# Optimization experiments

Hardware: AMD Instinct MI355X
Metric: run time of the kernel (lower is better)

## Reference

```python
import jax, jax.numpy as jnp
import numpy as np

HIDDEN = 768
HEADS = 12
HEAD_DIM = HIDDEN // HEADS  # 64


def setup_inputs() -> dict:
    key = jax.random.key(0)
    k1, k2, k3 = jax.random.split(key, 3)
    B, N, C = 64, 197, HIDDEN
    hidden_states = jax.random.normal(k1, (B, N, C), dtype=jnp.float32)
    # qkv Linear: weight [C, 3C] (stored transposed for x @ W), bias [3C]
    w_qkv = jax.random.normal(k2, (C, 3 * C), dtype=jnp.float32) * (1.0 / np.sqrt(C))
    b_qkv = jax.random.normal(k3, (3 * C,), dtype=jnp.float32) * 0.02
    return {"hidden_states": hidden_states, "w_qkv": w_qkv, "b_qkv": b_qkv}


def reference(hidden_states, w_qkv, b_qkv):
    B, N, C = hidden_states.shape
    scale = HEAD_DIM ** -0.5
    qkv = hidden_states @ w_qkv + b_qkv                      # [B, N, 3C]
    qkv = qkv.reshape(B, N, 3, HEADS, HEAD_DIM)
    qkv = jnp.transpose(qkv, (2, 0, 3, 1, 4))                # [3, B, H, N, d]
    q, k, v = qkv[0], qkv[1], qkv[2]
    scores = jnp.einsum("bhqd,bhkd->bhqk", q, k) * scale     # [B, H, N, N]
    probs = jax.nn.softmax(scores, axis=-1)
    # dropout is identity in eval mode (p=0.0)
    ctx = jnp.einsum("bhqk,bhkd->bhqd", probs, v)            # [B, H, N, d]
    ctx = jnp.transpose(ctx, (0, 2, 1, 3)).reshape(B, N, C)  # [B, N, C]
    return ctx
```

## Files before the change

kernel.cpp:

```cpp
#include <hip/hip_runtime.h>

#define M_ROWS 12608
#define K_DIM  768
#define XB_ELEMS (12800*768)

typedef __bf16 bf16x8 __attribute__((ext_vector_type(8)));
typedef float  f32x4  __attribute__((ext_vector_type(4)));

__device__ __forceinline__ unsigned short f2bf(float f) {
    unsigned u = __builtin_bit_cast(unsigned, f);
    u += 0x7fffu + ((u >> 16) & 1u);
    return (unsigned short)(u >> 16);
}

__device__ __forceinline__ void gll16(const unsigned short* g, unsigned short* l) {
    __builtin_amdgcn_global_load_lds(
        (const __attribute__((address_space(1))) unsigned int*)g,
        (__attribute__((address_space(3))) unsigned int*)l, 16, 0, 0);
}

__global__ __launch_bounds__(256) void prep_kernel(
        const float* __restrict__ X, unsigned short* __restrict__ Xb,
        const float* __restrict__ W, unsigned short* __restrict__ Wt) {
    __shared__ float tile[32][33];
    const int bid = blockIdx.x;
    if (bid < 4800) {
        size_t base = ((size_t)bid * 256 + threadIdx.x) * 8;
        if (base >= (size_t)M_ROWS * K_DIM) {
            *(ushort4*)(Xb + base) = (ushort4){0, 0, 0, 0};
            *(ushort4*)(Xb + base + 4) = (ushort4){0, 0, 0, 0};
            return;
        }
        float4 a = *(const float4*)(X + base);
        float4 b = *(const float4*)(X + base + 4);
        ushort4 lo, hi;
        lo.x = f2bf(a.x); lo.y = f2bf(a.y); lo.z = f2bf(a.z); lo.w = f2bf(a.w);
        hi.x = f2bf(b.x); hi.y = f2bf(b.y); hi.z = f2bf(b.z); hi.w = f2bf(b.w);
        *(ushort4*)(Xb + base) = lo;
        *(ushort4*)(Xb + base + 4) = hi;
        return;
    }
    const int b2 = bid - 4800;
    const int n0 = (b2 % 72) * 32, k0 = (b2 / 72) * 32;
    const int tx = threadIdx.x & 31, ty = threadIdx.x >> 5;
#pragma unroll
    for (int i = 0; i < 4; ++i)
        tile[ty + i * 8][tx] = W[(size_t)(k0 + ty + i * 8) * 2304 + n0 + tx];
    __syncthreads();
#pragma unroll
    for (int i = 0; i < 4; ++i)
        Wt[(size_t)(n0 + ty + i * 8) * K_DIM + k0 + tx] = f2bf(tile[tx][ty + i * 8]);
}

__global__ __launch_bounds__(512, 2) void fused_kernel(
        const unsigned short* __restrict__ Xb, const unsigned short* __restrict__ Wt,
        const float* __restrict__ bias, float* __restrict__ out) {
    __shared__ __align__(16) unsigned short L[70864];

    const int t = threadIdx.x;
    const int w = t >> 6, lane = t & 63, quad = lane >> 4, l16 = lane & 15;
    const int wrow0 = (w >> 1) * 64;
    const int wcol0 = (w & 1) * 96;

    const int lin = blockIdx.x;
    const int wg = (lin & 7) * 96 + (lin >> 3);
    const int bb = wg / 12, h = wg - bb * 12;

    const unsigned short* XbB = Xb + (size_t)(bb * 197) * K_DIM;

    const unsigned short* sgp[4];
    int sof[4];
    const int nst = (w < 4) ? 4 : 3;
    const int bstride = (w < 4) ? 8192 : 6144;
    if (w < 4) {
#pragma unroll
        for (int s = 0; s < 4; ++s) {
            sgp[s] = XbB + (size_t)(s * 64 + lane) * K_DIM + w * 8;
            sof[s] = w * 2048 + s * 512;
        }
    } else {
#pragma unroll
        for (int s = 0; s < 3; ++s) {
            const int idx = (w - 4) * 3 + s;
            const int kc = idx & 3, grp = idx >> 2;
            sgp[s] = Wt + (size_t)(grp * 768 + h * 64 + lane) * K_DIM + kc * 8;
            sof[s] = 16384 + kc * 1536 + grp * 512;
        }
        sgp[3] = sgp[0]; sof[3] = sof[0];
    }

    f32x4 acc[4][6];
#pragma unroll
    for (int i = 0; i < 4; ++i)
#pragma unroll
        for (int j = 0; j < 6; ++j) acc[i][j] = (f32x4){0.f, 0.f, 0.f, 0.f};

#pragma unroll
    for (int s = 0; s < 4; ++s)
        if (s < nst) gll16(sgp[s], &L[sof[s]]);
    asm volatile("s_waitcnt vmcnt(0)" ::: "memory");
    __builtin_amdgcn_s_barrier();
    asm volatile("" ::: "memory");

#pragma unroll 2
    for (int kt = 0; kt < 24; ++kt) {
        const int cur = kt & 1, nxt = cur ^ 1;
        const int sk = (kt + 1 < 24 ? kt + 1 : 0) * 32;

#pragma unroll
        for (int s = 0; s < 4; ++s)
            if (s < nst) gll16(sgp[s] + sk, &L[sof[s] + nxt * bstride]);

        const unsigned short* Ab = &L[cur * 8192];
        const unsigned short* Bb = &L[16384 + cur * 6144];
        bf16x8 af[4], bq[6];
#pragma unroll
        for (int i = 0; i < 4; ++i)
            af[i] = *(const bf16x8*)&Ab[quad * 2048 + (wrow0 + i * 16 + l16) * 8];
#pragma unroll
        for (int j = 0; j < 6; ++j)
            bq[j] = *(const bf16x8*)&Bb[quad * 1536 + (wcol0 + j * 16 + l16) * 8];

#pragma unroll
        for (int i = 0; i < 4; ++i)
#pragma unroll
            for (int j = 0; j < 6; ++j)
                acc[i][j] = __builtin_amdgcn_mfma_f32_16x16x32_bf16(af[i], bq[j], acc[i][j], 0, 0, 0);

        asm volatile("s_waitcnt vmcnt(0)" ::: "memory");
        __builtin_amdgcn_s_barrier();
        asm volatile("" ::: "memory");
    }

    unsigned short* Qs = &L[28672];
    unsigned short* Ks = &L[42856];
    unsigned short* Vt = &L[57040];
    unsigned short* Ps = &L[0];

#pragma unroll
    for (int j = 0; j < 6; ++j) {
        const int gnr = wcol0 + j * 16 + l16;
        const int which = gnr >> 6, d = gnr & 63;
        const float bv = bias[which * 768 + h * 64 + d];
#pragma unroll
        for (int i = 0; i < 4; ++i) {
            const int rowb = wrow0 + i * 16 + quad * 4;
#pragma unroll
            for (int r = 0; r < 4; ++r) {
                const int row = rowb + r;
                if (row >= 197) continue;
                const float val = acc[i][j][r] + bv;
                if (which == 0)      Qs[row * 72 + d] = f2bf(val * 0.125f);
                else if (which == 1) Ks[row * 72 + d] = f2bf(val);
                else                 Vt[d * 216 + row] = f2bf(val);
            }
        }
    }
    for (int idx = t; idx < 64 * 19; idx += 512) {
        int d = idx / 19, c = 197 + idx - d * 19;
        Vt[d * 216 + c] = 0;
    }
    __syncthreads();

    unsigned short* Pw = Ps + w * (16 * 136);

    for (int tile = w; tile < 13; tile += 8) {
        int rq = tile * 16 + l16;
        int tokq = rq < 197 ? rq : 196;
        bf16x8 aq0 = *(const bf16x8*)&Qs[tokq * 72 + quad * 8];
        bf16x8 aq1 = *(const bf16x8*)&Qs[tokq * 72 + 32 + quad * 8];

        f32x4 s[13];
        __builtin_amdgcn_s_setprio(1);
#pragma unroll
        for (int c = 0; c < 13; ++c) {
            int krow = c * 16 + l16;
            if (krow > 196) krow = 196;
            bf16x8 kb0 = *(const bf16x8*)&Ks[krow * 72 + quad * 8];
            bf16x8 kb1 = *(const bf16x8*)&Ks[krow * 72 + 32 + quad * 8];
            f32x4 zz = (f32x4){0.f, 0.f, 0.f, 0.f};
            zz = __builtin_amdgcn_mfma_f32_16x16x32_bf16(aq0, kb0, zz, 0, 0, 0);
            zz = __builtin_amdgcn_mfma_f32_16x16x32_bf16(aq1, kb1, zz, 0, 0, 0);
            s[c] = zz;
        }
        __builtin_amdgcn_s_setprio(0);
        if (l16 >= 5) { s[12][0] = -1e30f; s[12][1] = -1e30f; s[12][2] = -1e30f; s[12][3] = -1e30f; }

        float mx[4], lsum[4];
#pragma unroll
        for (int r = 0; r < 4; ++r) {
            float m = s[0][r];
#pragma unroll
            for (int c = 1; c < 13; ++c) m = fmaxf(m, s[c][r]);
#pragma unroll
            for (int d = 1; d < 16; d <<= 1) m = fmaxf(m, __shfl_xor(m, d));
            mx[r] = m;
            lsum[r] = 0.f;
        }
#pragma unroll
        for (int c = 0; c < 13; ++c)
#pragma unroll
            for (int r = 0; r < 4; ++r) {
                float p = __expf(s[c][r] - mx[r]);
                s[c][r] = p;
                lsum[r] += p;
            }
#pragma unroll
        for (int r = 0; r < 4; ++r)
#pragma unroll
            for (int d = 1; d < 16; d <<= 1) lsum[r] += __shfl_xor(lsum[r], d);

        f32x4 o[4];
#pragma unroll
        for (int j = 0; j < 4; ++j) o[j] = (f32x4){0.f, 0.f, 0.f, 0.f};

#pragma unroll
        for (int c = 0; c < 8; ++c)
#pragma unroll
            for (int r = 0; r < 4; ++r)
                Pw[(quad * 4 + r) * 136 + c * 16 + l16] = f2bf(s[c][r]);
        __builtin_amdgcn_s_setprio(1);
#pragma unroll
        for (int kc = 0; kc < 4; ++kc) {
            int kof = kc * 32 + quad * 8;
            bf16x8 ap = *(const bf16x8*)&Pw[l16 * 136 + kof];
#pragma unroll
            for (int j = 0; j < 4; ++j) {
                bf16x8 bv = *(const bf16x8*)&Vt[(j * 16 + l16) * 216 + kof];
                o[j] = __builtin_amdgcn_mfma_f32_16x16x32_bf16(ap, bv, o[j], 0, 0, 0);
            }
        }
        __builtin_amdgcn_s_setprio(0);
#pragma unroll
        for (int r = 0; r < 4; ++r)
            Pw[(quad * 4 + r) * 136 + 80 + l16] = 0;
#pragma unroll
        for (int c = 8; c < 13; ++c)
#pragma unroll
            for (int r = 0; r < 4; ++r)
                Pw[(quad * 4 + r) * 136 + (c - 8) * 16 + l16] = f2bf(s[c][r]);
        __builtin_amdgcn_s_setprio(1);
#pragma unroll
        for (int kc = 0; kc < 3; ++kc) {
            int kofA = kc * 32 + quad * 8;
            int kofB = (kc == 2 && quad >= 2) ? 0 : kofA;
            bf16x8 ap = *(const bf16x8*)&Pw[l16 * 136 + kofA];
#pragma unroll
            for (int j = 0; j < 4; ++j) {
                bf16x8 bv = *(const bf16x8*)&Vt[(j * 16 + l16) * 216 + 128 + kofB];
                o[j] = __builtin_amdgcn_mfma_f32_16x16x32_bf16(ap, bv, o[j], 0, 0, 0);
            }
        }
        __builtin_amdgcn_s_setprio(0);

        int tokbase = tile * 16 + quad * 4;
#pragma unroll
        for (int r = 0; r < 4; ++r) {
            int tr = tokbase + r;
            if (tr >= 197) continue;
            float inv = 1.f / lsum[r];
#pragma unroll
            for (int j = 0; j < 4; ++j)
                out[((size_t)(bb * 197 + tr)) * 768 + h * 64 + j * 16 + l16] = o[j][r] * inv;
        }
    }
}

extern "C" void kernel_launch(void* const* d_in, const int* in_sizes, int n_in,
                              void* d_out, int out_size, void* d_ws, size_t ws_size,
                              hipStream_t stream) {
    const float* X    = (const float*)d_in[0];
    const float* W    = (const float*)d_in[1];
    const float* bias = (const float*)d_in[2];
    float* out = (float*)d_out;

    unsigned short* Xb = (unsigned short*)d_ws;
    unsigned short* Wt = (unsigned short*)d_ws + XB_ELEMS;

    prep_kernel<<<6528, 256, 0, stream>>>(X, Xb, W, Wt);
    fused_kernel<<<768, 512, 0, stream>>>(Xb, Wt, bias, out);
}
```

Baseline: 217.6 us.

## Pre-chunk bf16 X and W into LDS-tile order for contiguous async loads

The prep kernel now writes X and transposed W in a pre-tiled layout where each 512-element chunk matches one LDS staging slot for a given k-tile. The fused kernel's global_load_lds calls then read fully contiguous 1KB segments per wave instead of strided 16-byte pieces from rows of length 768. This is meant to improve DRAM and L2 access efficiency in the GEMM main loop, at the cost of a more complex prep pass with more blocks and some padded rows per batch.

New measurement: 201.2 us. 7.5% less time.

```diff
diff --git a/kernel.cpp b/kernel.cpp
--- a/kernel.cpp
+++ b/kernel.cpp
@@ -2,7 +2,8 @@
 
 #define M_ROWS 12608
 #define K_DIM  768
-#define XB_ELEMS (12800*768)
+#define XC_ELEMS (64*24*16*512)
+#define WC_ELEMS (12*24*12*512)
 
 typedef __bf16 bf16x8 __attribute__((ext_vector_type(8)));
 typedef float  f32x4  __attribute__((ext_vector_type(4)));
@@ -20,40 +21,54 @@
 }
 
 __global__ __launch_bounds__(256) void prep_kernel(
-        const float* __restrict__ X, unsigned short* __restrict__ Xb,
-        const float* __restrict__ W, unsigned short* __restrict__ Wt) {
+        const float* __restrict__ X, unsigned short* __restrict__ Xc,
+        const float* __restrict__ W, unsigned short* __restrict__ Wc) {
     __shared__ float tile[32][33];
     const int bid = blockIdx.x;
-    if (bid < 4800) {
-        size_t base = ((size_t)bid * 256 + threadIdx.x) * 8;
-        if (base >= (size_t)M_ROWS * K_DIM) {
-            *(ushort4*)(Xb + base) = (ushort4){0, 0, 0, 0};
-            *(ushort4*)(Xb + base + 4) = (ushort4){0, 0, 0, 0};
-            return;
-        }
-        float4 a = *(const float4*)(X + base);
-        float4 b = *(const float4*)(X + base + 4);
-        ushort4 lo, hi;
-        lo.x = f2bf(a.x); lo.y = f2bf(a.y); lo.z = f2bf(a.z); lo.w = f2bf(a.w);
-        hi.x = f2bf(b.x); hi.y = f2bf(b.y); hi.z = f2bf(b.z); hi.w = f2bf(b.w);
-        *(ushort4*)(Xb + base) = lo;
-        *(ushort4*)(Xb + base + 4) = hi;
+    const int t = threadIdx.x;
+    if (bid < 6144) {
+        const int cg = bid * 4 + (t >> 6);
+        const int lane = t & 63;
+        const int p = cg / 384, rem = cg - p * 384;
+        const int kt = rem >> 4, c = rem & 15;
+        const int kc = c >> 2, rg = c & 3;
+        const int grow = p * 197 + rg * 64 + lane;
+        uint4 u = (uint4){0, 0, 0, 0};
+        if (grow < M_ROWS) {
+            const float* src = X + (size_t)grow * K_DIM + kt * 32 + kc * 8;
+            float4 a = *(const float4*)src;
+            float4 b = *(const float4*)(src + 4);
+            u.x = f2bf(a.x) | ((unsigned)f2bf(a.y) << 16);
+            u.y = f2bf(a.z) | ((unsigned)f2bf(a.w) << 16);
+            u.z = f2bf(b.x) | ((unsigned)f2bf(b.y) << 16);
+            u.w = f2bf(b.z) | ((unsigned)f2bf(b.w) << 16);
+        }
+        *(uint4*)(Xc + (size_t)cg * 512 + lane * 8) = u;
         return;
     }
-    const int b2 = bid - 4800;
+    const int b2 = bid - 6144;
     const int n0 = (b2 % 72) * 32, k0 = (b2 / 72) * 32;
-    const int tx = threadIdx.x & 31, ty = threadIdx.x >> 5;
+    const int tx = t & 31, ty = t >> 5;
 #pragma unroll
     for (int i = 0; i < 4; ++i)
         tile[ty + i * 8][tx] = W[(size_t)(k0 + ty + i * 8) * 2304 + n0 + tx];
     __syncthreads();
-#pragma unroll
-    for (int i = 0; i < 4; ++i)
-        Wt[(size_t)(n0 + ty + i * 8) * K_DIM + k0 + tx] = f2bf(tile[tx][ty + i * 8]);
+    if (t < 128) {
+        const int kc = t >> 5, tx2 = t & 31;
+        const int grp = n0 / 768, remn = n0 - grp * 768;
+        const int h = remn >> 6, lh = remn & 63;
+        const int kt = k0 >> 5;
+        uint4 u;
+        u.x = f2bf(tile[kc * 8 + 0][tx2]) | ((unsigned)f2bf(tile[kc * 8 + 1][tx2]) << 16);
+        u.y = f2bf(tile[kc * 8 + 2][tx2]) | ((unsigned)f2bf(tile[kc * 8 + 3][tx2]) << 16);
+        u.z = f2bf(tile[kc * 8 + 4][tx2]) | ((unsigned)f2bf(tile[kc * 8 + 5][tx2]) << 16);
+        u.w = f2bf(tile[kc * 8 + 6][tx2]) | ((unsigned)f2bf(tile[kc * 8 + 7][tx2]) << 16);
+        *(uint4*)(Wc + (size_t)(((h * 24 + kt) * 12) + kc * 3 + grp) * 512 + (lh + tx2) * 8) = u;
+    }
 }
 
 __global__ __launch_bounds__(512, 2) void fused_kernel(
-        const unsigned short* __restrict__ Xb, const unsigned short* __restrict__ Wt,
+        const unsigned short* __restrict__ Xc, const unsigned short* __restrict__ Wc,
         const float* __restrict__ bias, float* __restrict__ out) {
     __shared__ __align__(16) unsigned short L[70864];
 
@@ -66,25 +81,24 @@
     const int wg = (lin & 7) * 96 + (lin >> 3);
     const int bb = wg / 12, h = wg - bb * 12;
 
-    const unsigned short* XbB = Xb + (size_t)(bb * 197) * K_DIM;
-
     const unsigned short* sgp[4];
     int sof[4];
     const int nst = (w < 4) ? 4 : 3;
     const int bstride = (w < 4) ? 8192 : 6144;
+    const int kstride = (w < 4) ? 8192 : 6144;
     if (w < 4) {
 #pragma unroll
         for (int s = 0; s < 4; ++s) {
-            sgp[s] = XbB + (size_t)(s * 64 + lane) * K_DIM + w * 8;
-            sof[s] = w * 2048 + s * 512;
+            sgp[s] = Xc + ((size_t)(bb * 24) * 16 + w * 4 + s) * 512 + lane * 8;
+            sof[s] = (w * 4 + s) * 512;
         }
     } else {
 #pragma unroll
         for (int s = 0; s < 3; ++s) {
             const int idx = (w - 4) * 3 + s;
             const int kc = idx & 3, grp = idx >> 2;
-            sgp[s] = Wt + (size_t)(grp * 768 + h * 64 + lane) * K_DIM + kc * 8;
-            sof[s] = 16384 + kc * 1536 + grp * 512;
+            sgp[s] = Wc + ((size_t)(h * 24) * 12 + kc * 3 + grp) * 512 + lane * 8;
+            sof[s] = 16384 + (kc * 3 + grp) * 512;
         }
         sgp[3] = sgp[0]; sof[3] = sof[0];
     }
@@ -105,7 +119,7 @@
 #pragma unroll 2
     for (int kt = 0; kt < 24; ++kt) {
         const int cur = kt & 1, nxt = cur ^ 1;
-        const int sk = (kt + 1 < 24 ? kt + 1 : 0) * 32;
+        const int sk = (kt + 1 < 24 ? kt + 1 : 0) * kstride;
 
 #pragma unroll
         for (int s = 0; s < 4; ++s)
@@ -274,9 +288,9 @@
     const float* bias = (const float*)d_in[2];
     float* out = (float*)d_out;
 
-    unsigned short* Xb = (unsigned short*)d_ws;
-    unsigned short* Wt = (unsigned short*)d_ws + XB_ELEMS;
-
-    prep_kernel<<<6528, 256, 0, stream>>>(X, Xb, W, Wt);
-    fused_kernel<<<768, 512, 0, stream>>>(Xb, Wt, bias, out);
-}
+    unsigned short* Xc = (unsigned short*)d_ws;
+    unsigned short* Wc = (unsigned short*)d_ws + XC_ELEMS;
+
+    prep_kernel<<<7872, 256, 0, stream>>>(X, Xc, W, Wc);
+    fused_kernel<<<768, 512, 0, stream>>>(Xc, Wc, bias, out);
+}
```
